# Optimization experiments

Hardware: AMD Instinct MI355X
Metric: run time of the kernel (lower is better)

Reference implementation:

```python
import jax, jax.numpy as jnp
import numpy as np

EMBED_DIM = 512
NUM_HEADS = 8
HEAD_DIM = EMBED_DIM // NUM_HEADS
GRID = 48
BATCH = 8


def _locality_bias(grid_h, grid_w):
    # normalised negative squared L2 distances between patch centres, in [-1, 0]
    gy, gx = jnp.meshgrid(jnp.linspace(0.0, 1.0, grid_h),
                          jnp.linspace(0.0, 1.0, grid_w), indexing='ij')
    coords = jnp.stack([gy.reshape(-1), gx.reshape(-1)], axis=-1)  # (N, 2)
    diff = coords[None, :, :] - coords[:, None, :]                 # (N, N, 2)
    dist2 = jnp.sum(diff * diff, axis=-1)                          # (N, N)
    return -dist2 / jnp.max(dist2)


def setup_inputs() -> dict:
    key = jax.random.key(0)
    k_x, k_qkv, k_pw, k_pb, k_t, k_lw = jax.random.split(key, 6)
    N = GRID * GRID
    x = jax.random.normal(k_x, (BATCH, N, EMBED_DIM), dtype=jnp.float32)
    # torch nn.Linear weights are (out_features, in_features)
    qkv_w = jax.random.normal(k_qkv, (3 * EMBED_DIM, EMBED_DIM), dtype=jnp.float32) * 0.02
    proj_w = jax.random.normal(k_pw, (EMBED_DIM, EMBED_DIM), dtype=jnp.float32) * 0.02
    proj_b = jax.random.normal(k_pb, (EMBED_DIM,), dtype=jnp.float32) * 0.02
    init_temp = float(np.log(HEAD_DIM ** (-0.5)))
    temperature = init_temp + 0.02 * jax.random.normal(k_t, (NUM_HEADS, 1, 1), dtype=jnp.float32)
    locality_weight = 0.1 + 0.02 * jax.random.normal(k_lw, (NUM_HEADS,), dtype=jnp.float32)
    return {
        'x': x,
        'qkv_w': qkv_w,
        'proj_w': proj_w,
        'proj_b': proj_b,
        'temperature': temperature,
        'locality_weight': locality_weight,
        'grid_h': GRID,
        'grid_w': GRID,
    }


def reference(x, qkv_w, proj_w, proj_b, temperature, locality_weight, grid_h, grid_w):
    B, N, C = x.shape
    H = temperature.shape[0]
    D = C // H
    # qkv projection (no bias): (B, N, 3C) -> (3, B, H, N, D)
    qkv = (x @ qkv_w.T).reshape(B, N, 3, H, D)
    qkv = jnp.transpose(qkv, (2, 0, 3, 1, 4))
    q, k, v = qkv[0], qkv[1], qkv[2]              # each (B, H, N, D)
    scale = jnp.exp(temperature)                  # (H, 1, 1) learnable per-head temp
    attn = jnp.einsum('bhqd,bhkd->bhqk', q, k) * scale[None]
    loc = _locality_bias(grid_h, grid_w)          # (N, N), values in [-1, 0]
    attn = attn + locality_weight[None, :, None, None] * loc[None, None]
    attn = jax.nn.softmax(attn, axis=-1)          # dropout is identity (p=0 / eval)
    out = jnp.einsum('bhqk,bhkd->bhqd', attn, v)  # (B, H, N, D)
    out = jnp.transpose(out, (0, 2, 1, 3)).reshape(B, N, C)
    return out @ proj_w.T + proj_b
```

## Files before the change

### kernel.cpp

```cpp
#include <hip/hip_runtime.h>

typedef unsigned int   uint_ma   __attribute__((may_alias));
typedef unsigned short ushort_ma __attribute__((may_alias));
typedef float          float_ma  __attribute__((may_alias));
typedef __bf16 bf16x8 __attribute__((ext_vector_type(8)));
typedef float f32x4 __attribute__((ext_vector_type(4)));
typedef uint_ma u32x4 __attribute__((ext_vector_type(4)));
typedef uint_ma u32x2 __attribute__((ext_vector_type(2)));
typedef ushort_ma u16x4 __attribute__((ext_vector_type(4)));

#define BATCH 8
#define NTOK 2304
#define CDIM 512
#define NH 8
#define HD 64
#define MROWS (BATCH * NTOK)
#define LOG2E 1.44269504088896f

constexpr size_t N_X  = (size_t)BATCH * NTOK * CDIM;
constexpr size_t N_WQ = (size_t)3 * CDIM * CDIM;
constexpr size_t N_WP = (size_t)CDIM * CDIM;
constexpr size_t OFF_XO = 0;
constexpr size_t OFF_WQ = OFF_XO + N_X;
constexpr size_t OFF_WP = OFF_WQ + N_WQ;
constexpr size_t OFF_Q  = OFF_WP + N_WP;
constexpr size_t OFF_K  = OFF_Q + N_X;
constexpr size_t OFF_V  = OFF_K + N_X;
constexpr size_t CV8 = (N_X + N_WQ + N_WP) / 8;

__device__ __forceinline__ float bf2f(unsigned short h) {
  unsigned int u = ((unsigned int)h) << 16;
  return __builtin_bit_cast(float, u);
}
__device__ __forceinline__ unsigned short f2bf(float f) {
  unsigned int u = __builtin_bit_cast(unsigned int, f);
  u += 0x7fffu + ((u >> 16) & 1u);
  return (unsigned short)(u >> 16);
}

__device__ __forceinline__ void gload16(const void* g, void* l) {
  __builtin_amdgcn_global_load_lds(
      (const __attribute__((address_space(1))) void*)g,
      (__attribute__((address_space(3))) void*)l, 16, 0, 0);
}

__global__ __launch_bounds__(256) void convert3(
    const float* __restrict__ s0, const float* __restrict__ s1,
    const float* __restrict__ s2, ushort_ma* __restrict__ base) {
  const size_t gid = (size_t)blockIdx.x * blockDim.x + threadIdx.x;
  const size_t stride = (size_t)gridDim.x * blockDim.x;
  for (size_t i = gid; i < CV8; i += stride) {
    size_t r = i;
    const float* src;
    size_t doff;
    if (r < N_X / 8) { src = s0; doff = OFF_XO; }
    else if ((r -= N_X / 8) < N_WQ / 8) { src = s1; doff = OFF_WQ; }
    else { r -= N_WQ / 8; src = s2; doff = OFF_WP; }
    const f32x4* fw = (const f32x4*)(src + r * 8);
    const f32x4 a = fw[0], b = fw[1];
    u16x4 lo, hi;
#pragma unroll
    for (int j = 0; j < 4; j++) { lo[j] = f2bf(a[j]); hi[j] = f2bf(b[j]); }
    ushort_ma* dst = base + doff + r * 8;
    *(u16x4*)dst = lo;
    *(u16x4*)(dst + 4) = hi;
  }
}

template <int MODE>
__global__ __launch_bounds__(256, 3) void gemm_bt(
    const ushort_ma* __restrict__ A, const ushort_ma* __restrict__ W,
    const float* __restrict__ aux,
    unsigned short* __restrict__ o0,
    unsigned short* __restrict__ o1,
    unsigned short* __restrict__ o2)
{
  __shared__ __align__(16) ushort_ma As[2][128][32];
  __shared__ __align__(16) ushort_ma Bs[2][128][32];
  const int K = CDIM;
  const int m0 = blockIdx.x * 128;
  const int n0 = blockIdx.y * 128;
  const int t = threadIdx.x;
  const int lane = t & 63;
  const int w = t >> 6;
  const int wm = (w >> 1) * 64, wn = (w & 1) * 64;
  const int lr = lane & 15, lq = lane >> 4;

  const int srow = w * 16 + (lane >> 2);
  const int scg = (lane & 3) ^ ((srow >> 1) & 3);
  const ushort_ma* Ag0 = A + (size_t)(m0 + srow) * K + scg * 8;
  const ushort_ma* Ag1 = Ag0 + (size_t)64 * K;
  const ushort_ma* Bg0 = W + (size_t)(n0 + srow) * K + scg * 8;
  const ushort_ma* Bg1 = Bg0 + (size_t)64 * K;

  const f32x4 fz = {0.f, 0.f, 0.f, 0.f};
  f32x4 acc[4][4];
#pragma unroll
  for (int i = 0; i < 4; i++)
#pragma unroll
    for (int j = 0; j < 4; j++) acc[i][j] = fz;

  auto issue = [&](int kt, int buf) {
    const int k0 = kt * 32;
    gload16(Ag0 + k0, (void*)&As[buf][w * 16][0]);
    gload16(Ag1 + k0, (void*)&As[buf][64 + w * 16][0]);
    gload16(Bg0 + k0, (void*)&Bs[buf][w * 16][0]);
    gload16(Bg1 + k0, (void*)&Bs[buf][64 + w * 16][0]);
  };

  issue(0, 0);
  const int colf = 8 * (lq ^ ((lr >> 1) & 3));

  for (int kt = 0; kt < 16; kt++) {
    const int buf = kt & 1;
    __syncthreads();
    if (kt < 15) issue(kt + 1, buf ^ 1);
    bf16x8 af[4], bfr[4];
#pragma unroll
    for (int i = 0; i < 4; i++)
      af[i] = __builtin_bit_cast(bf16x8, *(const u32x4*)(&As[buf][wm + i * 16 + lr][colf]));
#pragma unroll
    for (int j = 0; j < 4; j++)
      bfr[j] = __builtin_bit_cast(bf16x8, *(const u32x4*)(&Bs[buf][wn + j * 16 + lr][colf]));
#pragma unroll
    for (int i = 0; i < 4; i++)
#pragma unroll
      for (int j = 0; j < 4; j++)
        acc[i][j] = __builtin_amdgcn_mfma_f32_16x16x32_bf16(bfr[j], af[i], acc[i][j], 0, 0, 0);
  }

  if (MODE == 0) {
#pragma unroll
    for (int j = 0; j < 4; j++) {
      const int gcb = n0 + wn + j * 16 + lq * 4;
      const int which = gcb >> 9;
      const int h = (gcb >> 6) & 7;
      const int db = gcb & 63;
      const float sc = (which == 0) ? __expf(aux[h]) * LOG2E : 1.0f;
      unsigned short* dst = (which == 0) ? o0 : o1;
#pragma unroll
      for (int i = 0; i < 4; i++) {
        const int gm = m0 + wm + i * 16 + lr;
        const int b = gm / NTOK;
        const int np = gm - b * NTOK;
        if (which == 2) {
#pragma unroll
          for (int r = 0; r < 4; r++)
            o2[((size_t)((b * NH + h) * HD + db + r)) * NTOK + np] = f2bf(acc[i][j][r]);
        } else {
          u16x4 pk;
#pragma unroll
          for (int r = 0; r < 4; r++) pk[r] = f2bf(acc[i][j][r] * sc);
          *(u16x4*)(dst + ((size_t)((b * NH + h) * NTOK + np)) * HD + db) = pk;
        }
      }
    }
  } else {
    float_ma* outf = (float_ma*)o0;
#pragma unroll
    for (int j = 0; j < 4; j++) {
      const int gcb = n0 + wn + j * 16 + lq * 4;
      const f32x4 bv4 = *(const f32x4*)(aux + gcb);
#pragma unroll
      for (int i = 0; i < 4; i++) {
        const int gm = m0 + wm + i * 16 + lr;
        f32x4 ov;
#pragma unroll
        for (int r = 0; r < 4; r++) ov[r] = acc[i][j][r] + bv4[r];
        *(f32x4*)(outf + (size_t)gm * CDIM + gcb) = ov;
      }
    }
  }
}

__global__ __launch_bounds__(256, 3) void attn_kernel(
    const ushort_ma* __restrict__ Qg,
    const ushort_ma* __restrict__ Kg,
    const ushort_ma* __restrict__ Vg,
    const float* __restrict__ lwp,
    unsigned short* __restrict__ Og)
{
  __shared__ __align__(16) ushort_ma Ks[128][72];
  __shared__ __align__(16) ushort_ma Vs[64][136];
  __shared__ __align__(16) ushort_ma Ps[4][32][36];

  const int bh = blockIdx.y;
  const int b = bh >> 3, h = bh & 7;
  const int q0 = blockIdx.x * 128;
  const int t = threadIdx.x;
  const int lane = t & 63;
  const int w = t >> 6;
  const int lr = lane & 15, lq = lane >> 4;

  const ushort_ma* Qw = Qg + ((size_t)bh * NTOK + q0 + (size_t)w * 32) * HD;
  bf16x8 aQ[2][2];
#pragma unroll
  for (int mi = 0; mi < 2; mi++)
#pragma unroll
    for (int ks = 0; ks < 2; ks++)
      aQ[mi][ks] = __builtin_bit_cast(
          bf16x8, *(const u32x4*)(Qw + (size_t)(mi * 16 + lr) * HD + ks * 32 + lq * 8));

  const float cb2 = -0.5f * LOG2E * lwp[h];
  bf16x8 aQb[2];
#pragma unroll
  for (int mi = 0; mi < 2; mi++) {
    const int qrow = q0 + w * 32 + mi * 16 + lr;
    const int yy = qrow / 48;
    const int xx = qrow - yy * 48;
    const float fy = (float)yy * (1.0f / 47.0f);
    const float fx = (float)xx * (1.0f / 47.0f);
    u32x4 v = {0u, 0u, 0u, 0u};
    if (lq == 0) {
      v[0] = (unsigned int)f2bf(fy) | ((unsigned int)f2bf(fx) << 16);
      v[1] = (unsigned int)f2bf(fy * fy + fx * fx) | (0x3F80u << 16);
    }
    aQb[mi] = __builtin_bit_cast(bf16x8, v);
  }

  const u32x4 onesU = {0x3F803F80u, 0x3F803F80u, 0x3F803F80u, 0x3F803F80u};
  const bf16x8 bOnes = __builtin_bit_cast(bf16x8, onesU);

  const f32x4 fz = {0.f, 0.f, 0.f, 0.f};
  f32x4 accO[2][4];
  f32x4 accL[2];
#pragma unroll
  for (int mi = 0; mi < 2; mi++) {
    accL[mi] = fz;
#pragma unroll
    for (int nd = 0; nd < 4; nd++) accO[mi][nd] = fz;
  }

  const ushort_ma* Kb = Kg + (size_t)bh * NTOK * HD;
  const ushort_ma* Vb = Vg + (size_t)bh * HD * NTOK;

  for (int kt = 0; kt < 18; kt++) {
    const int kv0 = kt * 128;
    __syncthreads();
    {
      u32x4 kc[4], vc[4];
#pragma unroll
      for (int it = 0; it < 4; it++) {
        const int q = t + it * 256;
        kc[it] = *(const u32x4*)(Kb + (size_t)(kv0 + (q >> 3)) * HD + (q & 7) * 8);
        vc[it] = *(const u32x4*)(Vb + (size_t)(q >> 4) * NTOK + kv0 + (q & 15) * 8);
      }
#pragma unroll
      for (int it = 0; it < 4; it++) {
        const int q = t + it * 256;
        *(u32x4*)(&Ks[q >> 3][(q & 7) * 8]) = kc[it];
        *(u32x4*)(&Vs[q >> 4][(q & 15) * 8]) = vc[it];
      }
    }
    if (t < 128) {
      const int kv = kv0 + t;
      const int yy = kv / 48;
      const int xx = kv - yy * 48;
      const float fy = (float)yy * (1.0f / 47.0f);
      const float fx = (float)xx * (1.0f / 47.0f);
      u32x4 bv;
      bv[0] = (unsigned int)f2bf(-2.0f * cb2 * fy) |
              ((unsigned int)f2bf(-2.0f * cb2 * fx) << 16);
      bv[1] = (unsigned int)f2bf(cb2) |
              ((unsigned int)f2bf(cb2 * (fy * fy + fx * fx)) << 16);
      bv[2] = 0u;
      bv[3] = 0u;
      *(u32x4*)(&Ks[t][64]) = bv;
    }
    __syncthreads();

#pragma unroll
    for (int c = 0; c < 4; c++) {
      f32x4 s2[2][2] = {{fz, fz}, {fz, fz}};
      __builtin_amdgcn_s_setprio(1);
#pragma unroll
      for (int e2 = 0; e2 < 2; e2++) {
        const int ni = 2 * c + e2;
#pragma unroll
        for (int ks = 0; ks < 2; ks++) {
          const bf16x8 bK = __builtin_bit_cast(
              bf16x8, *(const u32x4*)(&Ks[ni * 16 + lr][ks * 32 + lq * 8]));
#pragma unroll
          for (int mi = 0; mi < 2; mi++)
            s2[mi][e2] = __builtin_amdgcn_mfma_f32_16x16x32_bf16(bK, aQ[mi][ks], s2[mi][e2], 0, 0, 0);
        }
        const bf16x8 bKb = __builtin_bit_cast(
            bf16x8, *(const u32x4*)(&Ks[ni * 16 + lr][64]));
#pragma unroll
        for (int mi = 0; mi < 2; mi++)
          s2[mi][e2] = __builtin_amdgcn_mfma_f32_16x16x32_bf16(bKb, aQb[mi], s2[mi][e2], 0, 0, 0);
      }
      __builtin_amdgcn_s_setprio(0);
#pragma unroll
      for (int mi = 0; mi < 2; mi++)
#pragma unroll
        for (int e2 = 0; e2 < 2; e2++) {
          unsigned int pb[4];
#pragma unroll
          for (int r = 0; r < 4; r++) {
            const float p = __builtin_amdgcn_exp2f(s2[mi][e2][r]);
            pb[r] = (__builtin_bit_cast(unsigned int, p) >> 16) & 0xFFFFu;
          }
          u32x2 pk;
          pk[0] = pb[0] | (pb[1] << 16);
          pk[1] = pb[2] | (pb[3] << 16);
          *(u32x2*)(&Ps[w][mi * 16 + lr][e2 * 16 + lq * 4]) = pk;
        }
      __asm__ volatile("s_waitcnt lgkmcnt(0)" ::: "memory");
      bf16x8 aP[2];
#pragma unroll
      for (int mi = 0; mi < 2; mi++)
        aP[mi] = __builtin_bit_cast(
            bf16x8, *(const u32x4*)(&Ps[w][mi * 16 + lr][lq * 8]));
      __builtin_amdgcn_s_setprio(1);
#pragma unroll
      for (int nd = 0; nd < 4; nd++) {
        const bf16x8 bV = __builtin_bit_cast(
            bf16x8, *(const u32x4*)(&Vs[nd * 16 + lr][c * 32 + lq * 8]));
#pragma unroll
        for (int mi = 0; mi < 2; mi++)
          accO[mi][nd] = __builtin_amdgcn_mfma_f32_16x16x32_bf16(aP[mi], bV, accO[mi][nd], 0, 0, 0);
      }
#pragma unroll
      for (int mi = 0; mi < 2; mi++)
        accL[mi] = __builtin_amdgcn_mfma_f32_16x16x32_bf16(aP[mi], bOnes, accL[mi], 0, 0, 0);
      __builtin_amdgcn_s_setprio(0);
    }
  }

#pragma unroll
  for (int mi = 0; mi < 2; mi++) {
    f32x4 inv;
#pragma unroll
    for (int r = 0; r < 4; r++) inv[r] = 1.0f / accL[mi][r];
#pragma unroll
    for (int nd = 0; nd < 4; nd++)
#pragma unroll
      for (int r = 0; r < 4; r++) {
        const int np = q0 + w * 32 + mi * 16 + lq * 4 + r;
        Og[((size_t)(b * NTOK + np)) * CDIM + h * HD + nd * 16 + lr] =
            f2bf(accO[mi][nd][r] * inv[r]);
      }
  }
}

extern "C" void kernel_launch(void* const* d_in, const int* in_sizes, int n_in,
                              void* d_out, int out_size, void* d_ws, size_t ws_size,
                              hipStream_t stream) {
  const float* x      = (const float*)d_in[0];
  const float* qkv_w  = (const float*)d_in[1];
  const float* proj_w = (const float*)d_in[2];
  const float* proj_b = (const float*)d_in[3];
  const float* temp   = (const float*)d_in[4];
  const float* lw     = (const float*)d_in[5];

  ushort_ma* base = (ushort_ma*)d_ws;
  ushort_ma* XB  = base + OFF_XO;
  ushort_ma* WQB = base + OFF_WQ;
  ushort_ma* WPB = base + OFF_WP;
  ushort_ma* Q   = base + OFF_Q;
  ushort_ma* Kt  = base + OFF_K;
  ushort_ma* Vt  = base + OFF_V;
  ushort_ma* O   = XB;

  convert3<<<1024, 256, 0, stream>>>(x, qkv_w, proj_w, base);
  gemm_bt<0><<<dim3(MROWS / 128, 1536 / 128), 256, 0, stream>>>(
      XB, WQB, temp, (unsigned short*)Q, (unsigned short*)Kt, (unsigned short*)Vt);
  attn_kernel<<<dim3(NTOK / 128, BATCH * NH), 256, 0, stream>>>(
      Q, Kt, Vt, lw, (unsigned short*)O);
  gemm_bt<1><<<dim3(MROWS / 128, CDIM / 128), 256, 0, stream>>>(
      O, WPB, proj_b, (unsigned short*)d_out, nullptr, nullptr);
}
```

Baseline: 285.6 us.

## Software-pipeline QK and PV MFMAs with double-buffered P, remap blocks for XCD locality

The attention inner loop now computes the next chunk's S scores before issuing the current chunk's PV MFMAs, and does the exp/pack after them. P sits in a double-buffered LDS tile so the softmax exp work can overlap with matrix-core work. The grid is also flattened to 1D, and block IDs are remapped so consecutive blocks on the same XCD share a batch-head, which should improve L2 reuse of K/V. The cost is more LDS for P and more live registers, which may lower occupancy.

```diff
diff --git a/kernel.cpp b/kernel.cpp
--- a/kernel.cpp
+++ b/kernel.cpp
@@ -182,11 +182,13 @@
 {
   __shared__ __align__(16) ushort_ma Ks[128][72];
   __shared__ __align__(16) ushort_ma Vs[64][136];
-  __shared__ __align__(16) ushort_ma Ps[4][32][36];
-
-  const int bh = blockIdx.y;
+  __shared__ __align__(16) ushort_ma Ps[4][2][32][36];
+
+  const int orig = blockIdx.x;
+  const int v = (orig & 7) * 144 + (orig >> 3);
+  const int bh = v / 18;
+  const int q0 = (v - bh * 18) * 128;
   const int b = bh >> 3, h = bh & 7;
-  const int q0 = blockIdx.x * 128;
   const int t = threadIdx.x;
   const int lane = t & 63;
   const int w = t >> 6;
@@ -210,12 +212,12 @@
     const int xx = qrow - yy * 48;
     const float fy = (float)yy * (1.0f / 47.0f);
     const float fx = (float)xx * (1.0f / 47.0f);
-    u32x4 v = {0u, 0u, 0u, 0u};
+    u32x4 vv = {0u, 0u, 0u, 0u};
     if (lq == 0) {
-      v[0] = (unsigned int)f2bf(fy) | ((unsigned int)f2bf(fx) << 16);
-      v[1] = (unsigned int)f2bf(fy * fy + fx * fx) | (0x3F80u << 16);
-    }
-    aQb[mi] = __builtin_bit_cast(bf16x8, v);
+      vv[0] = (unsigned int)f2bf(fy) | ((unsigned int)f2bf(fx) << 16);
+      vv[1] = (unsigned int)f2bf(fy * fy + fx * fx) | (0x3F80u << 16);
+    }
+    aQb[mi] = __builtin_bit_cast(bf16x8, vv);
   }
 
   const u32x4 onesU = {0x3F803F80u, 0x3F803F80u, 0x3F803F80u, 0x3F803F80u};
@@ -233,6 +235,49 @@
 
   const ushort_ma* Kb = Kg + (size_t)bh * NTOK * HD;
   const ushort_ma* Vb = Vg + (size_t)bh * HD * NTOK;
+
+  auto computeS = [&](int cc, f32x4 (&out)[2][2]) {
+#pragma unroll
+    for (int mi = 0; mi < 2; mi++) { out[mi][0] = fz; out[mi][1] = fz; }
+    __builtin_amdgcn_s_setprio(1);
+#pragma unroll
+    for (int e2 = 0; e2 < 2; e2++) {
+      const int ni = 2 * cc + e2;
+#pragma unroll
+      for (int ks = 0; ks < 2; ks++) {
+        const bf16x8 bK = __builtin_bit_cast(
+            bf16x8, *(const u32x4*)(&Ks[ni * 16 + lr][ks * 32 + lq * 8]));
+#pragma unroll
+        for (int mi = 0; mi < 2; mi++)
+          out[mi][e2] = __builtin_amdgcn_mfma_f32_16x16x32_bf16(bK, aQ[mi][ks], out[mi][e2], 0, 0, 0);
+      }
+      const bf16x8 bKb = __builtin_bit_cast(
+          bf16x8, *(const u32x4*)(&Ks[ni * 16 + lr][64]));
+#pragma unroll
+      for (int mi = 0; mi < 2; mi++)
+        out[mi][e2] = __builtin_amdgcn_mfma_f32_16x16x32_bf16(bKb, aQb[mi], out[mi][e2], 0, 0, 0);
+    }
+    __builtin_amdgcn_s_setprio(0);
+  };
+
+  auto packP = [&](int cc, f32x4 (&sin)[2][2]) {
+    const int bf = cc & 1;
+#pragma unroll
+    for (int mi = 0; mi < 2; mi++)
+#pragma unroll
+      for (int e2 = 0; e2 < 2; e2++) {
+        unsigned int pb[4];
+#pragma unroll
+        for (int r = 0; r < 4; r++) {
+          const float p = __builtin_amdgcn_exp2f(sin[mi][e2][r]);
+          pb[r] = (__builtin_bit_cast(unsigned int, p) >> 16) & 0xFFFFu;
+        }
+        u32x2 pk;
+        pk[0] = pb[0] | (pb[1] << 16);
+        pk[1] = pb[2] | (pb[3] << 16);
+        *(u32x2*)(&Ps[w][bf][mi * 16 + lr][e2 * 16 + lq * 4]) = pk;
+      }
+  };
 
   for (int kt = 0; kt < 18; kt++) {
     const int kv0 = kt * 128;
@@ -269,49 +314,18 @@
     }
     __syncthreads();
 
+    f32x4 s2[2][2];
+    computeS(0, s2);
+    packP(0, s2);
 #pragma unroll
     for (int c = 0; c < 4; c++) {
-      f32x4 s2[2][2] = {{fz, fz}, {fz, fz}};
-      __builtin_amdgcn_s_setprio(1);
-#pragma unroll
-      for (int e2 = 0; e2 < 2; e2++) {
-        const int ni = 2 * c + e2;
-#pragma unroll
-        for (int ks = 0; ks < 2; ks++) {
-          const bf16x8 bK = __builtin_bit_cast(
-              bf16x8, *(const u32x4*)(&Ks[ni * 16 + lr][ks * 32 + lq * 8]));
-#pragma unroll
-          for (int mi = 0; mi < 2; mi++)
-            s2[mi][e2] = __builtin_amdgcn_mfma_f32_16x16x32_bf16(bK, aQ[mi][ks], s2[mi][e2], 0, 0, 0);
-        }
-        const bf16x8 bKb = __builtin_bit_cast(
-            bf16x8, *(const u32x4*)(&Ks[ni * 16 + lr][64]));
-#pragma unroll
-        for (int mi = 0; mi < 2; mi++)
-          s2[mi][e2] = __builtin_amdgcn_mfma_f32_16x16x32_bf16(bKb, aQb[mi], s2[mi][e2], 0, 0, 0);
-      }
-      __builtin_amdgcn_s_setprio(0);
-#pragma unroll
-      for (int mi = 0; mi < 2; mi++)
-#pragma unroll
-        for (int e2 = 0; e2 < 2; e2++) {
-          unsigned int pb[4];
-#pragma unroll
-          for (int r = 0; r < 4; r++) {
-            const float p = __builtin_amdgcn_exp2f(s2[mi][e2][r]);
-            pb[r] = (__builtin_bit_cast(unsigned int, p) >> 16) & 0xFFFFu;
-          }
-          u32x2 pk;
-          pk[0] = pb[0] | (pb[1] << 16);
-          pk[1] = pb[2] | (pb[3] << 16);
-          *(u32x2*)(&Ps[w][mi * 16 + lr][e2 * 16 + lq * 4]) = pk;
-        }
+      if (c < 3) computeS(c + 1, s2);
       __asm__ volatile("s_waitcnt lgkmcnt(0)" ::: "memory");
       bf16x8 aP[2];
 #pragma unroll
       for (int mi = 0; mi < 2; mi++)
         aP[mi] = __builtin_bit_cast(
-            bf16x8, *(const u32x4*)(&Ps[w][mi * 16 + lr][lq * 8]));
+            bf16x8, *(const u32x4*)(&Ps[w][c & 1][mi * 16 + lr][lq * 8]));
       __builtin_amdgcn_s_setprio(1);
 #pragma unroll
       for (int nd = 0; nd < 4; nd++) {
@@ -325,6 +339,7 @@
       for (int mi = 0; mi < 2; mi++)
         accL[mi] = __builtin_amdgcn_mfma_f32_16x16x32_bf16(aP[mi], bOnes, accL[mi], 0, 0, 0);
       __builtin_amdgcn_s_setprio(0);
+      if (c < 3) packP(c + 1, s2);
     }
   }
 
@@ -366,7 +381,7 @@
   convert3<<<1024, 256, 0, stream>>>(x, qkv_w, proj_w, base);
   gemm_bt<0><<<dim3(MROWS / 128, 1536 / 128), 256, 0, stream>>>(
       XB, WQB, temp, (unsigned short*)Q, (unsigned short*)Kt, (unsigned short*)Vt);
-  attn_kernel<<<dim3(NTOK / 128, BATCH * NH), 256, 0, stream>>>(
+  attn_kernel<<<dim3((NTOK / 128) * BATCH * NH), 256, 0, stream>>>(
       Q, Kt, Vt, lw, (unsigned short*)O);
   gemm_bt<1><<<dim3(MROWS / 128, CDIM / 128), 256, 0, stream>>>(
       O, WPB, proj_b, (unsigned short*)d_out, nullptr, nullptr);
```

Result: slower. 300.6 us (+5.3%).
